# Kernel tuning notes

Measured on AMD Instinct MI355X. Metric: run time of the kernel, lower is better.

Reference implementation:

```python
import jax, jax.numpy as jnp
import numpy as np

NUM_EXPERTS = 8
TOP_K = 2
HIDDEN = 2048
INTER = 2816  # 2*INTER = 5632 fused gate+up
NUM_TOKENS = 8192


def setup_inputs() -> dict:
    key = jax.random.key(0)
    k1, k2, k3, k4 = jax.random.split(key, 4)
    hidden_states = jax.random.normal(k1, (NUM_TOKENS, HIDDEN), dtype=jnp.float32)
    gate_w = jax.random.normal(k2, (NUM_EXPERTS, HIDDEN), dtype=jnp.float32) * 0.02
    w13 = jax.random.normal(k3, (NUM_EXPERTS, 2 * INTER, HIDDEN), dtype=jnp.float32) * 0.02
    w2 = jax.random.normal(k4, (NUM_EXPERTS, HIDDEN, INTER), dtype=jnp.float32) * 0.02
    return {"hidden_states": hidden_states, "gate_w": gate_w, "w13": w13, "w2": w2}


def reference(hidden_states, gate_w, w13, w2):
    x = hidden_states  # [T, H]
    # Gate: ReplicatedLinear (no bias) -> router logits [T, E]
    router_logits = jnp.einsum('th,eh->te', x, gate_w)
    probs = jax.nn.softmax(router_logits, axis=-1)
    # top-k routing, renormalize=False: use softmax probs directly
    topk_vals, topk_idx = jax.lax.top_k(probs, TOP_K)  # [T, K]
    # combine weights [T, E]: sum of one-hot(topk_idx) * topk_vals
    cw = jnp.sum(jax.nn.one_hot(topk_idx, NUM_EXPERTS, dtype=x.dtype) * topk_vals[..., None], axis=1)
    # Dense per-expert grouped GEMM, masked combine (E is small and fixed)
    out = jnp.zeros_like(x)
    for e in range(NUM_EXPERTS):
        gu = jnp.einsum('th,ih->ti', x, w13[e])          # [T, 2I]
        g, u = gu[:, :INTER], gu[:, INTER:]
        h = jax.nn.silu(g) * u                            # SiLU-gated
        y = jnp.einsum('ti,hi->th', h, w2[e])             # [T, H]
        out = out + cw[:, e:e + 1] * y
    return out
```

## Files before the change

kernel.cpp:

```cpp
#include <hip/hip_runtime.h>
#include <stdint.h>
#include <stddef.h>

#define NE 8
#define HIDDEN 2048
#define INTER 2816
#define NT 8192
#define NROWS (NT * 2)

typedef __bf16 bf16x8 __attribute__((ext_vector_type(8)));
typedef float f32x4 __attribute__((ext_vector_type(4)));

__device__ __forceinline__ unsigned short f2bf(float f) {
  union { float f; uint32_t u; } v; v.f = f;
  uint32_t r = v.u + 0x7FFFu + ((v.u >> 16) & 1u);
  return (unsigned short)(r >> 16);
}

__device__ __forceinline__ void async16(const void* g, const unsigned short* lds_ptr) {
  __builtin_amdgcn_global_load_lds(
      (const __attribute__((address_space(1))) uint32_t*)g,
      (__attribute__((address_space(3))) uint32_t*)lds_ptr,
      16, 0, 0);
}

__global__ void cvt_kernel(const float4* __restrict__ src, ushort4* __restrict__ dst) {
  size_t i = (size_t)blockIdx.x * blockDim.x + threadIdx.x;
  float4 v = src[i];
  ushort4 o;
  o.x = f2bf(v.x); o.y = f2bf(v.y); o.z = f2bf(v.z); o.w = f2bf(v.w);
  dst[i] = o;
}

__global__ __launch_bounds__(256) void router_kernel(
    const float* __restrict__ x, const float* __restrict__ gw,
    int* __restrict__ top_e, float* __restrict__ top_w, int* __restrict__ counts) {
  int t = blockIdx.x * 4 + (threadIdx.x >> 6);
  int lane = threadIdx.x & 63;
  const float* xr = x + (size_t)t * HIDDEN;
  float acc[NE];
#pragma unroll
  for (int e = 0; e < NE; ++e) acc[e] = 0.f;
  for (int kb = 0; kb < HIDDEN; kb += 64) {
    float xv = xr[kb + lane];
#pragma unroll
    for (int e = 0; e < NE; ++e) acc[e] += xv * gw[e * HIDDEN + kb + lane];
  }
#pragma unroll
  for (int e = 0; e < NE; ++e) {
#pragma unroll
    for (int off = 32; off > 0; off >>= 1) acc[e] += __shfl_xor(acc[e], off, 64);
  }
  if (lane == 0) {
    float mx = acc[0];
#pragma unroll
    for (int e = 1; e < NE; ++e) mx = fmaxf(mx, acc[e]);
    float p[NE];
    float s = 0.f;
#pragma unroll
    for (int e = 0; e < NE; ++e) { p[e] = expf(acc[e] - mx); s += p[e]; }
    int e1 = 0;
#pragma unroll
    for (int e = 1; e < NE; ++e) if (p[e] > p[e1]) e1 = e;
    int e2 = (e1 == 0) ? 1 : 0;
#pragma unroll
    for (int e = 0; e < NE; ++e) if (e != e1 && p[e] > p[e2]) e2 = e;
    float inv = 1.f / s;
    top_e[2 * t] = e1; top_e[2 * t + 1] = e2;
    top_w[2 * t] = p[e1] * inv; top_w[2 * t + 1] = p[e2] * inv;
    atomicAdd(&counts[e1], 1);
    atomicAdd(&counts[e2], 1);
  }
}

__global__ void scan_kernel(const int* __restrict__ counts, int* __restrict__ offs) {
  if (threadIdx.x == 0) {
    int s = 0;
    for (int e = 0; e < NE; ++e) { offs[e] = s; s += counts[e]; }
    offs[NE] = s;
  }
}

__global__ void fill_kernel(const int* __restrict__ top_e, const float* __restrict__ top_w,
                            const int* __restrict__ offs, int* __restrict__ fillc,
                            int* __restrict__ row_tok, float* __restrict__ row_w,
                            int* __restrict__ row_of) {
  int t = blockIdx.x * 256 + threadIdx.x;
#pragma unroll
  for (int j = 0; j < 2; ++j) {
    int e = top_e[2 * t + j];
    int slot = atomicAdd(&fillc[e], 1);
    int row = offs[e] + slot;
    row_tok[row] = t;
    row_w[row] = top_w[2 * t + j];
    row_of[2 * t + j] = row;
  }
}

__global__ __launch_bounds__(256, 2) void gemm1_kernel(
    const unsigned short* __restrict__ xb, const unsigned short* __restrict__ w13b,
    const int* __restrict__ row_tok, const int* __restrict__ offs,
    unsigned short* __restrict__ hbuf) {
  __shared__ __align__(16) unsigned short smem[3 * 4096];
  const int e = blockIdx.z, mt = blockIdx.y, nt = blockIdx.x;
  const int row0 = offs[e];
  const int cnt = offs[e + 1] - row0;
  if (mt * 128 >= cnt) return;
  const int tid = threadIdx.x;
  const int ldr = tid >> 2;
  const int sw_st = (ldr >> 1) & 3;
  const int ldc = ((tid & 3) ^ sw_st) * 8;
  size_t abase[2], bgbase[2], bubase[2];
#pragma unroll
  for (int i = 0; i < 2; ++i) {
    int grow = mt * 128 + i * 64 + ldr;
    int rr = row0 + (grow < cnt ? grow : cnt - 1);
    abase[i] = (size_t)row_tok[rr] * HIDDEN + ldc;
    int n = nt * 128 + i * 64 + ldr;
    bgbase[i] = ((size_t)e * 2 * INTER + n) * HIDDEN + ldc;
    bubase[i] = ((size_t)e * 2 * INTER + INTER + n) * HIDDEN + ldc;
  }
  const int wv = tid >> 6, wm = wv & 1, wn = wv >> 1;
  const int l = tid & 63, lm = l & 15, lq = l >> 4;
  const int sw = (lm >> 1) & 3;
  f32x4 accg[4][4], accu[4][4];
#pragma unroll
  for (int i = 0; i < 4; ++i)
#pragma unroll
    for (int j = 0; j < 4; ++j) {
      accg[i][j] = (f32x4){0.f, 0.f, 0.f, 0.f};
      accu[i][j] = (f32x4){0.f, 0.f, 0.f, 0.f};
    }
  for (int k0 = 0; k0 < HIDDEN; k0 += 32) {
    __syncthreads();
    async16(xb + abase[0] + k0, smem + tid * 8);
    async16(xb + abase[1] + k0, smem + 2048 + tid * 8);
    async16(w13b + bgbase[0] + k0, smem + 4096 + tid * 8);
    async16(w13b + bgbase[1] + k0, smem + 6144 + tid * 8);
    async16(w13b + bubase[0] + k0, smem + 8192 + tid * 8);
    async16(w13b + bubase[1] + k0, smem + 10240 + tid * 8);
    __syncthreads();
    bf16x8 af[4], bgf[4], buf[4];
#pragma unroll
    for (int i = 0; i < 4; ++i) {
      af[i] = *(const bf16x8*)(smem + (wm * 64 + i * 16 + lm) * 32 + ((lq ^ sw) * 8));
      bgf[i] = *(const bf16x8*)(smem + 4096 + (wn * 64 + i * 16 + lm) * 32 + ((lq ^ sw) * 8));
      buf[i] = *(const bf16x8*)(smem + 8192 + (wn * 64 + i * 16 + lm) * 32 + ((lq ^ sw) * 8));
    }
#pragma unroll
    for (int i = 0; i < 4; ++i)
#pragma unroll
      for (int j = 0; j < 4; ++j) {
        accg[i][j] = __builtin_amdgcn_mfma_f32_16x16x32_bf16(af[i], bgf[j], accg[i][j], 0, 0, 0);
        accu[i][j] = __builtin_amdgcn_mfma_f32_16x16x32_bf16(af[i], buf[j], accu[i][j], 0, 0, 0);
      }
  }
#pragma unroll
  for (int i = 0; i < 4; ++i) {
#pragma unroll
    for (int r = 0; r < 4; ++r) {
      int grow = mt * 128 + wm * 64 + i * 16 + lq * 4 + r;
      if (grow < cnt) {
        size_t hrow = (size_t)(row0 + grow) * INTER + nt * 128 + wn * 64 + lm;
#pragma unroll
        for (int j = 0; j < 4; ++j) {
          float g = accg[i][j][r], u = accu[i][j][r];
          float sg = g / (1.f + expf(-g));
          hbuf[hrow + j * 16] = f2bf(sg * u);
        }
      }
    }
  }
}

__global__ __launch_bounds__(256, 2) void gemm2_kernel(
    const unsigned short* __restrict__ hbuf, const unsigned short* __restrict__ w2b,
    const float* __restrict__ row_w, const int* __restrict__ offs,
    float* __restrict__ ybuf) {
  __shared__ __align__(16) unsigned short smem[2 * 4096];
  const int e = blockIdx.z, mt = blockIdx.y, nt = blockIdx.x;
  const int row0 = offs[e];
  const int cnt = offs[e + 1] - row0;
  if (mt * 128 >= cnt) return;
  const int tid = threadIdx.x;
  const int ldr = tid >> 2;
  const int sw_st = (ldr >> 1) & 3;
  const int ldc = ((tid & 3) ^ sw_st) * 8;
  size_t abase[2], bbase[2];
#pragma unroll
  for (int i = 0; i < 2; ++i) {
    int grow = mt * 128 + i * 64 + ldr;
    int rr = row0 + (grow < cnt ? grow : cnt - 1);
    abase[i] = (size_t)rr * INTER + ldc;
    int n = nt * 128 + i * 64 + ldr;
    bbase[i] = ((size_t)e * HIDDEN + n) * INTER + ldc;
  }
  const int wv = tid >> 6, wm = wv & 1, wn = wv >> 1;
  const int l = tid & 63, lm = l & 15, lq = l >> 4;
  const int sw = (lm >> 1) & 3;
  f32x4 acc[4][4];
#pragma unroll
  for (int i = 0; i < 4; ++i)
#pragma unroll
    for (int j = 0; j < 4; ++j) acc[i][j] = (f32x4){0.f, 0.f, 0.f, 0.f};
  for (int k0 = 0; k0 < INTER; k0 += 32) {
    __syncthreads();
    async16(hbuf + abase[0] + k0, smem + tid * 8);
    async16(hbuf + abase[1] + k0, smem + 2048 + tid * 8);
    async16(w2b + bbase[0] + k0, smem + 4096 + tid * 8);
    async16(w2b + bbase[1] + k0, smem + 6144 + tid * 8);
    __syncthreads();
    bf16x8 af[4], bf[4];
#pragma unroll
    for (int i = 0; i < 4; ++i) {
      af[i] = *(const bf16x8*)(smem + (wm * 64 + i * 16 + lm) * 32 + ((lq ^ sw) * 8));
      bf[i] = *(const bf16x8*)(smem + 4096 + (wn * 64 + i * 16 + lm) * 32 + ((lq ^ sw) * 8));
    }
#pragma unroll
    for (int i = 0; i < 4; ++i)
#pragma unroll
      for (int j = 0; j < 4; ++j)
        acc[i][j] = __builtin_amdgcn_mfma_f32_16x16x32_bf16(af[i], bf[j], acc[i][j], 0, 0, 0);
  }
#pragma unroll
  for (int i = 0; i < 4; ++i) {
#pragma unroll
    for (int r = 0; r < 4; ++r) {
      int grow = mt * 128 + wm * 64 + i * 16 + lq * 4 + r;
      if (grow < cnt) {
        int rr = row0 + grow;
        float w = row_w[rr];
        float* yrow = ybuf + (size_t)rr * HIDDEN + nt * 128 + wn * 64 + lm;
#pragma unroll
        for (int j = 0; j < 4; ++j) yrow[j * 16] = w * acc[i][j][r];
      }
    }
  }
}

__global__ __launch_bounds__(256) void combine_kernel(
    const float* __restrict__ ybuf, const int* __restrict__ row_of,
    float* __restrict__ out) {
  int t = blockIdx.x;
  int r0 = row_of[2 * t], r1 = row_of[2 * t + 1];
  const float4* y0 = (const float4*)(ybuf + (size_t)r0 * HIDDEN);
  const float4* y1 = (const float4*)(ybuf + (size_t)r1 * HIDDEN);
  float4* o = (float4*)(out + (size_t)t * HIDDEN);
#pragma unroll
  for (int it = 0; it < 2; ++it) {
    int c = it * 256 + threadIdx.x;
    float4 a = y0[c], b = y1[c];
    o[c] = make_float4(a.x + b.x, a.y + b.y, a.z + b.z, a.w + b.w);
  }
}

extern "C" void kernel_launch(void* const* d_in, const int* in_sizes, int n_in,
                              void* d_out, int out_size, void* d_ws, size_t ws_size,
                              hipStream_t stream) {
  const float* x = (const float*)d_in[0];
  const float* gw = (const float*)d_in[1];
  const float* w13 = (const float*)d_in[2];
  const float* w2 = (const float*)d_in[3];
  float* out = (float*)d_out;
  char* ws = (char*)d_ws;

  int* counts = (int*)(ws + 0);
  int* fillc = (int*)(ws + 32);
  int* offs = (int*)(ws + 64);
  int* top_e = (int*)(ws + 1024);
  float* top_w = (float*)(ws + 66560);
  int* row_tok = (int*)(ws + 132096);
  float* row_w = (float*)(ws + 197632);
  int* row_of = (int*)(ws + 263168);
  unsigned short* xb = (unsigned short*)(ws + 328704);
  unsigned short* w13b = (unsigned short*)(ws + 33883136);
  float* ybuf = (float*)(ws + 33883136);
  unsigned short* w2b = (unsigned short*)(ws + 218432512);
  unsigned short* hb = (unsigned short*)(ws + 310707200);

  hipMemsetAsync(ws, 0, 1024, stream);

  cvt_kernel<<<16384, 256, 0, stream>>>((const float4*)x, (ushort4*)xb);
  cvt_kernel<<<90112, 256, 0, stream>>>((const float4*)w13, (ushort4*)w13b);
  cvt_kernel<<<45056, 256, 0, stream>>>((const float4*)w2, (ushort4*)w2b);

  router_kernel<<<2048, 256, 0, stream>>>(x, gw, top_e, top_w, counts);
  scan_kernel<<<1, 64, 0, stream>>>(counts, offs);
  fill_kernel<<<32, 256, 0, stream>>>(top_e, top_w, offs, fillc, row_tok, row_w, row_of);

  gemm1_kernel<<<dim3(22, 64, 8), 256, 0, stream>>>(xb, w13b, row_tok, offs, hb);
  gemm2_kernel<<<dim3(16, 64, 8), 256, 0, stream>>>(hb, w2b, row_w, offs, ybuf);
  combine_kernel<<<8192, 256, 0, stream>>>(ybuf, row_of, out);
}
```

Measured before the change: 1.721 ms.

## Double-buffer MoE GEMMs with 512-thread 256-row tiles and interleaved async prefetch

Both expert GEMMs move from 256-thread 128x128 tiles with a single LDS buffer to 512-thread blocks covering 256 rows and a double-buffered BK=64 LDS pipeline. Global-to-LDS async loads for the next k-tile are issued between MFMA phases, using explicit vmcnt waits, raw s_barrier, sched_barrier and setprio instead of syncthreads. gemm2 also widens to 256 output columns per block, and gemm1 splits its gate and up MFMA phases. The goal is to hide load latency and raise data reuse per block, at the cost of much more LDS (128KB per block) and register pressure, which can lower occupancy.

```diff
diff --git a/kernel.cpp b/kernel.cpp
--- a/kernel.cpp
+++ b/kernel.cpp
@@ -97,32 +97,33 @@
   }
 }
 
-__global__ __launch_bounds__(256, 2) void gemm1_kernel(
+__global__ __launch_bounds__(512, 2) void gemm1_kernel(
     const unsigned short* __restrict__ xb, const unsigned short* __restrict__ w13b,
     const int* __restrict__ row_tok, const int* __restrict__ offs,
     unsigned short* __restrict__ hbuf) {
-  __shared__ __align__(16) unsigned short smem[3 * 4096];
+  __shared__ __align__(16) unsigned short smem[2][2][16384];
   const int e = blockIdx.z, mt = blockIdx.y, nt = blockIdx.x;
   const int row0 = offs[e];
   const int cnt = offs[e + 1] - row0;
-  if (mt * 128 >= cnt) return;
+  if (mt * 256 >= cnt) return;
   const int tid = threadIdx.x;
-  const int ldr = tid >> 2;
-  const int sw_st = (ldr >> 1) & 3;
-  const int ldc = ((tid & 3) ^ sw_st) * 8;
-  size_t abase[2], bgbase[2], bubase[2];
+
+  const int lrow = tid >> 2;
+  const int gch = ((tid & 3) ^ ((lrow >> 1) & 3)) * 8;
+  size_t aA[2];
 #pragma unroll
   for (int i = 0; i < 2; ++i) {
-    int grow = mt * 128 + i * 64 + ldr;
+    int grow = mt * 256 + i * 128 + lrow;
     int rr = row0 + (grow < cnt ? grow : cnt - 1);
-    abase[i] = (size_t)row_tok[rr] * HIDDEN + ldc;
-    int n = nt * 128 + i * 64 + ldr;
-    bgbase[i] = ((size_t)e * 2 * INTER + n) * HIDDEN + ldc;
-    bubase[i] = ((size_t)e * 2 * INTER + INTER + n) * HIDDEN + ldc;
-  }
-  const int wv = tid >> 6, wm = wv & 1, wn = wv >> 1;
+    aA[i] = (size_t)row_tok[rr] * HIDDEN + gch;
+  }
+  const size_t aBg = ((size_t)e * 2 * INTER + nt * 128 + lrow) * (size_t)HIDDEN + gch;
+  const size_t aBu = ((size_t)e * 2 * INTER + INTER + nt * 128 + lrow) * (size_t)HIDDEN + gch;
+
+  const int wv = tid >> 6, wm = wv >> 1, wn = wv & 1;
   const int l = tid & 63, lm = l & 15, lq = l >> 4;
-  const int sw = (lm >> 1) & 3;
+  const int loff = lm * 32 + ((lq ^ ((lm >> 1) & 3)) * 8);
+
   f32x4 accg[4][4], accu[4][4];
 #pragma unroll
   for (int i = 0; i < 4; ++i)
@@ -131,35 +132,77 @@
       accg[i][j] = (f32x4){0.f, 0.f, 0.f, 0.f};
       accu[i][j] = (f32x4){0.f, 0.f, 0.f, 0.f};
     }
-  for (int k0 = 0; k0 < HIDDEN; k0 += 32) {
-    __syncthreads();
-    async16(xb + abase[0] + k0, smem + tid * 8);
-    async16(xb + abase[1] + k0, smem + 2048 + tid * 8);
-    async16(w13b + bgbase[0] + k0, smem + 4096 + tid * 8);
-    async16(w13b + bgbase[1] + k0, smem + 6144 + tid * 8);
-    async16(w13b + bubase[0] + k0, smem + 8192 + tid * 8);
-    async16(w13b + bubase[1] + k0, smem + 10240 + tid * 8);
-    __syncthreads();
-    bf16x8 af[4], bgf[4], buf[4];
-#pragma unroll
-    for (int i = 0; i < 4; ++i) {
-      af[i] = *(const bf16x8*)(smem + (wm * 64 + i * 16 + lm) * 32 + ((lq ^ sw) * 8));
-      bgf[i] = *(const bf16x8*)(smem + 4096 + (wn * 64 + i * 16 + lm) * 32 + ((lq ^ sw) * 8));
-      buf[i] = *(const bf16x8*)(smem + 8192 + (wn * 64 + i * 16 + lm) * 32 + ((lq ^ sw) * 8));
-    }
-#pragma unroll
-    for (int i = 0; i < 4; ++i)
-#pragma unroll
-      for (int j = 0; j < 4; ++j) {
-        accg[i][j] = __builtin_amdgcn_mfma_f32_16x16x32_bf16(af[i], bgf[j], accg[i][j], 0, 0, 0);
-        accu[i][j] = __builtin_amdgcn_mfma_f32_16x16x32_bf16(af[i], buf[j], accu[i][j], 0, 0, 0);
+
+#define ST_A1(NB, KH, KT) do { \
+    size_t ko = (size_t)(KT) * 64 + (KH) * 32; \
+    async16(xb + aA[0] + ko, &smem[NB][KH][tid * 8]); \
+    async16(xb + aA[1] + ko, &smem[NB][KH][4096 + tid * 8]); } while (0)
+#define ST_B1(NB, KH, KT) do { \
+    size_t ko = (size_t)(KT) * 64 + (KH) * 32; \
+    async16(w13b + aBg + ko, &smem[NB][KH][8192 + tid * 8]); \
+    async16(w13b + aBu + ko, &smem[NB][KH][12288 + tid * 8]); } while (0)
+
+  ST_A1(0, 0, 0); ST_B1(0, 0, 0); ST_A1(0, 1, 0); ST_B1(0, 1, 0);
+  asm volatile("s_waitcnt vmcnt(4)" ::: "memory");
+  __builtin_amdgcn_s_barrier();
+
+  const int NTK = HIDDEN / 64;
+  for (int t = 0; t < NTK; ++t) {
+    const int b = t & 1, nb = b ^ 1;
+    const bool pf = (t + 1 < NTK);
+#pragma unroll
+    for (int kk = 0; kk < 2; ++kk) {
+      const unsigned short* sK = &smem[b][kk][0];
+      bf16x8 af[4], bfr[4];
+#pragma unroll
+      for (int i = 0; i < 4; ++i)
+        af[i] = *(const bf16x8*)(sK + (wm * 64 + i * 16) * 32 + loff);
+#pragma unroll
+      for (int j = 0; j < 4; ++j)
+        bfr[j] = *(const bf16x8*)(sK + (256 + wn * 64 + j * 16) * 32 + loff);
+      if (pf) ST_A1(nb, kk, t + 1);
+      __builtin_amdgcn_s_barrier();
+      asm volatile("s_waitcnt lgkmcnt(0)" ::: "memory");
+      __builtin_amdgcn_sched_barrier(0);
+      __builtin_amdgcn_s_setprio(1);
+#pragma unroll
+      for (int i = 0; i < 4; ++i)
+#pragma unroll
+        for (int j = 0; j < 4; ++j)
+          accg[i][j] = __builtin_amdgcn_mfma_f32_16x16x32_bf16(af[i], bfr[j], accg[i][j], 0, 0, 0);
+      __builtin_amdgcn_s_setprio(0);
+      __builtin_amdgcn_s_barrier();
+#pragma unroll
+      for (int j = 0; j < 4; ++j)
+        bfr[j] = *(const bf16x8*)(sK + (384 + wn * 64 + j * 16) * 32 + loff);
+      if (pf) ST_B1(nb, kk, t + 1);
+      if (kk == 0) {
+        if (pf) { asm volatile("s_waitcnt vmcnt(4)" ::: "memory"); }
+        else    { asm volatile("s_waitcnt vmcnt(0)" ::: "memory"); }
+      } else if (pf) {
+        asm volatile("s_waitcnt vmcnt(4)" ::: "memory");
       }
-  }
+      __builtin_amdgcn_s_barrier();
+      asm volatile("s_waitcnt lgkmcnt(0)" ::: "memory");
+      __builtin_amdgcn_sched_barrier(0);
+      __builtin_amdgcn_s_setprio(1);
+#pragma unroll
+      for (int i = 0; i < 4; ++i)
+#pragma unroll
+        for (int j = 0; j < 4; ++j)
+          accu[i][j] = __builtin_amdgcn_mfma_f32_16x16x32_bf16(af[i], bfr[j], accu[i][j], 0, 0, 0);
+      __builtin_amdgcn_s_setprio(0);
+      __builtin_amdgcn_s_barrier();
+    }
+  }
+#undef ST_A1
+#undef ST_B1
+
 #pragma unroll
   for (int i = 0; i < 4; ++i) {
 #pragma unroll
     for (int r = 0; r < 4; ++r) {
-      int grow = mt * 128 + wm * 64 + i * 16 + lq * 4 + r;
+      int grow = mt * 256 + wm * 64 + i * 16 + lq * 4 + r;
       if (grow < cnt) {
         size_t hrow = (size_t)(row0 + grow) * INTER + nt * 128 + wn * 64 + lm;
 #pragma unroll
@@ -173,66 +216,114 @@
   }
 }
 
-__global__ __launch_bounds__(256, 2) void gemm2_kernel(
+__global__ __launch_bounds__(512, 2) void gemm2_kernel(
     const unsigned short* __restrict__ hbuf, const unsigned short* __restrict__ w2b,
     const float* __restrict__ row_w, const int* __restrict__ offs,
     float* __restrict__ ybuf) {
-  __shared__ __align__(16) unsigned short smem[2 * 4096];
+  __shared__ __align__(16) unsigned short smem[2][2][16384];
   const int e = blockIdx.z, mt = blockIdx.y, nt = blockIdx.x;
   const int row0 = offs[e];
   const int cnt = offs[e + 1] - row0;
-  if (mt * 128 >= cnt) return;
+  if (mt * 256 >= cnt) return;
   const int tid = threadIdx.x;
-  const int ldr = tid >> 2;
-  const int sw_st = (ldr >> 1) & 3;
-  const int ldc = ((tid & 3) ^ sw_st) * 8;
-  size_t abase[2], bbase[2];
+
+  const int lrow = tid >> 2;
+  const int gch = ((tid & 3) ^ ((lrow >> 1) & 3)) * 8;
+  size_t aA[2], aB[2];
 #pragma unroll
   for (int i = 0; i < 2; ++i) {
-    int grow = mt * 128 + i * 64 + ldr;
+    int grow = mt * 256 + i * 128 + lrow;
     int rr = row0 + (grow < cnt ? grow : cnt - 1);
-    abase[i] = (size_t)rr * INTER + ldc;
-    int n = nt * 128 + i * 64 + ldr;
-    bbase[i] = ((size_t)e * HIDDEN + n) * INTER + ldc;
-  }
-  const int wv = tid >> 6, wm = wv & 1, wn = wv >> 1;
+    aA[i] = (size_t)rr * INTER + gch;
+    aB[i] = ((size_t)e * HIDDEN + nt * 256 + i * 128 + lrow) * (size_t)INTER + gch;
+  }
+
+  const int wv = tid >> 6, wm = wv >> 1, wn = wv & 1;
   const int l = tid & 63, lm = l & 15, lq = l >> 4;
-  const int sw = (lm >> 1) & 3;
-  f32x4 acc[4][4];
+  const int loff = lm * 32 + ((lq ^ ((lm >> 1) & 3)) * 8);
+
+  f32x4 acc[4][8];
 #pragma unroll
   for (int i = 0; i < 4; ++i)
 #pragma unroll
-    for (int j = 0; j < 4; ++j) acc[i][j] = (f32x4){0.f, 0.f, 0.f, 0.f};
-  for (int k0 = 0; k0 < INTER; k0 += 32) {
-    __syncthreads();
-    async16(hbuf + abase[0] + k0, smem + tid * 8);
-    async16(hbuf + abase[1] + k0, smem + 2048 + tid * 8);
-    async16(w2b + bbase[0] + k0, smem + 4096 + tid * 8);
-    async16(w2b + bbase[1] + k0, smem + 6144 + tid * 8);
-    __syncthreads();
-    bf16x8 af[4], bf[4];
-#pragma unroll
-    for (int i = 0; i < 4; ++i) {
-      af[i] = *(const bf16x8*)(smem + (wm * 64 + i * 16 + lm) * 32 + ((lq ^ sw) * 8));
-      bf[i] = *(const bf16x8*)(smem + 4096 + (wn * 64 + i * 16 + lm) * 32 + ((lq ^ sw) * 8));
-    }
-#pragma unroll
-    for (int i = 0; i < 4; ++i)
+    for (int j = 0; j < 8; ++j) acc[i][j] = (f32x4){0.f, 0.f, 0.f, 0.f};
+
+#define ST_A2(NB, KH, KT) do { \
+    size_t ko = (size_t)(KT) * 64 + (KH) * 32; \
+    async16(hbuf + aA[0] + ko, &smem[NB][KH][tid * 8]); \
+    async16(hbuf + aA[1] + ko, &smem[NB][KH][4096 + tid * 8]); } while (0)
+#define ST_B2(NB, KH, KT) do { \
+    size_t ko = (size_t)(KT) * 64 + (KH) * 32; \
+    async16(w2b + aB[0] + ko, &smem[NB][KH][8192 + tid * 8]); \
+    async16(w2b + aB[1] + ko, &smem[NB][KH][12288 + tid * 8]); } while (0)
+
+  ST_A2(0, 0, 0); ST_B2(0, 0, 0); ST_A2(0, 1, 0); ST_B2(0, 1, 0);
+  asm volatile("s_waitcnt vmcnt(4)" ::: "memory");
+  __builtin_amdgcn_s_barrier();
+
+  const int NTK = INTER / 64;
+  for (int t = 0; t < NTK; ++t) {
+    const int b = t & 1, nb = b ^ 1;
+    const bool pf = (t + 1 < NTK);
+#pragma unroll
+    for (int kk = 0; kk < 2; ++kk) {
+      const unsigned short* sK = &smem[b][kk][0];
+      bf16x8 af[4], bfr[4];
+#pragma unroll
+      for (int i = 0; i < 4; ++i)
+        af[i] = *(const bf16x8*)(sK + (wm * 64 + i * 16) * 32 + loff);
 #pragma unroll
       for (int j = 0; j < 4; ++j)
-        acc[i][j] = __builtin_amdgcn_mfma_f32_16x16x32_bf16(af[i], bf[j], acc[i][j], 0, 0, 0);
-  }
+        bfr[j] = *(const bf16x8*)(sK + (256 + wn * 128 + j * 16) * 32 + loff);
+      if (pf) ST_A2(nb, kk, t + 1);
+      __builtin_amdgcn_s_barrier();
+      asm volatile("s_waitcnt lgkmcnt(0)" ::: "memory");
+      __builtin_amdgcn_sched_barrier(0);
+      __builtin_amdgcn_s_setprio(1);
+#pragma unroll
+      for (int i = 0; i < 4; ++i)
+#pragma unroll
+        for (int j = 0; j < 4; ++j)
+          acc[i][j] = __builtin_amdgcn_mfma_f32_16x16x32_bf16(af[i], bfr[j], acc[i][j], 0, 0, 0);
+      __builtin_amdgcn_s_setprio(0);
+      __builtin_amdgcn_s_barrier();
+#pragma unroll
+      for (int j = 0; j < 4; ++j)
+        bfr[j] = *(const bf16x8*)(sK + (256 + wn * 128 + (j + 4) * 16) * 32 + loff);
+      if (pf) ST_B2(nb, kk, t + 1);
+      if (kk == 0) {
+        if (pf) { asm volatile("s_waitcnt vmcnt(4)" ::: "memory"); }
+        else    { asm volatile("s_waitcnt vmcnt(0)" ::: "memory"); }
+      } else if (pf) {
+        asm volatile("s_waitcnt vmcnt(4)" ::: "memory");
+      }
+      __builtin_amdgcn_s_barrier();
+      asm volatile("s_waitcnt lgkmcnt(0)" ::: "memory");
+      __builtin_amdgcn_sched_barrier(0);
+      __builtin_amdgcn_s_setprio(1);
+#pragma unroll
+      for (int i = 0; i < 4; ++i)
+#pragma unroll
+        for (int j = 0; j < 4; ++j)
+          acc[i][j + 4] = __builtin_amdgcn_mfma_f32_16x16x32_bf16(af[i], bfr[j], acc[i][j + 4], 0, 0, 0);
+      __builtin_amdgcn_s_setprio(0);
+      __builtin_amdgcn_s_barrier();
+    }
+  }
+#undef ST_A2
+#undef ST_B2
+
 #pragma unroll
   for (int i = 0; i < 4; ++i) {
 #pragma unroll
     for (int r = 0; r < 4; ++r) {
-      int grow = mt * 128 + wm * 64 + i * 16 + lq * 4 + r;
+      int grow = mt * 256 + wm * 64 + i * 16 + lq * 4 + r;
       if (grow < cnt) {
         int rr = row0 + grow;
         float w = row_w[rr];
-        float* yrow = ybuf + (size_t)rr * HIDDEN + nt * 128 + wn * 64 + lm;
-#pragma unroll
-        for (int j = 0; j < 4; ++j) yrow[j * 16] = w * acc[i][j][r];
+        float* yrow = ybuf + (size_t)rr * HIDDEN + nt * 256 + wn * 128 + lm;
+#pragma unroll
+        for (int j = 0; j < 8; ++j) yrow[j * 16] = w * acc[i][j][r];
       }
     }
   }
@@ -288,7 +379,7 @@
   scan_kernel<<<1, 64, 0, stream>>>(counts, offs);
   fill_kernel<<<32, 256, 0, stream>>>(top_e, top_w, offs, fillc, row_tok, row_w, row_of);
 
-  gemm1_kernel<<<dim3(22, 64, 8), 256, 0, stream>>>(xb, w13b, row_tok, offs, hb);
-  gemm2_kernel<<<dim3(16, 64, 8), 256, 0, stream>>>(hb, w2b, row_w, offs, ybuf);
+  gemm1_kernel<<<dim3(22, 32, 8), 512, 0, stream>>>(xb, w13b, row_tok, offs, hb);
+  gemm2_kernel<<<dim3(8, 32, 8), 512, 0, stream>>>(hb, w2b, row_w, offs, ybuf);
   combine_kernel<<<8192, 256, 0, stream>>>(ybuf, row_of, out);
 }
```

Measured after the change: 1.644 ms. 1.05x faster.
